# Optimization experiments

Hardware: AMD Instinct MI355X
Metric: run time of the kernel (lower is better)

Reference implementation:

```python
import jax, jax.numpy as jnp
import numpy as np

HIDDEN = 512

def setup_inputs() -> dict:
    key = jax.random.key(0)
    ks = jax.random.split(key, 6)
    B, T = 65536, 100
    scale = 0.1  # keep tanh MLP in a sane dynamic range
    return {
        "y0": jax.random.normal(ks[0], (B, 2), jnp.float32),
        "t_points": jnp.arange(T, dtype=jnp.float32) * 0.01,
        "W1": jax.random.normal(ks[1], (2, HIDDEN), jnp.float32) * scale,
        "b1": jnp.zeros((HIDDEN,), jnp.float32),
        "W2": jax.random.normal(ks[2], (HIDDEN, HIDDEN), jnp.float32) * scale,
        "b2": jnp.zeros((HIDDEN,), jnp.float32),
        "W3": jax.random.normal(ks[3], (HIDDEN, HIDDEN // 2), jnp.float32) * scale,
        "b3": jnp.zeros((HIDDEN // 2,), jnp.float32),
        "W4": jax.random.normal(ks[4], (HIDDEN // 2, 2), jnp.float32) * scale,
        "b4": jnp.zeros((2,), jnp.float32),
    }

def _mlp(y, W1, b1, W2, b2, W3, b3, W4, b4):
    # 4-layer tanh MLP: 2 -> H -> H -> H//2 -> 2 (t is unused in ODEFunc)
    h = jnp.tanh(y @ W1 + b1)
    h = jnp.tanh(h @ W2 + b2)
    h = jnp.tanh(h @ W3 + b3)
    return h @ W4 + b4

def reference(y0, t_points, W1, b1, W2, b2, W3, b3, W4, b4):
    f = lambda y: _mlp(y, W1, b1, W2, b2, W3, b3, W4, b4)
    dts = t_points[1:] - t_points[:-1]  # [T-1]

    def step(y, dt):
        k1 = f(y)
        k2 = f(y + k1 * (dt * 0.5))
        k3 = f(y + k2 * (dt * 0.5))
        k4 = f(y + k3 * dt)
        y_next = y + (dt / 6.0) * (k1 + 2.0 * k2 + 2.0 * k3 + k4)
        return y_next, y_next

    _, traj = jax.lax.scan(step, y0, dts)
    return jnp.concatenate([y0[None], traj], axis=0)  # [T, B, 2]
```

## Files before the change

### kernel.cpp

```cpp
#include <hip/hip_runtime.h>
#include <hip/hip_bf16.h>
#include <stdint.h>

using bfrag_t = __attribute__((ext_vector_type(8))) short;
using f32x16  = __attribute__((ext_vector_type(16))) float;

#define HID  512
#define H3   256
#define RB   64
#define NTH  512
#define KSC  2.885390081777927f

static __device__ __forceinline__ uint32_t bf16_rne(float f) {
    uint32_t u = __float_as_uint(f);
    return (u + 0x7fffu + ((u >> 16) & 1u)) >> 16;
}
static __device__ __forceinline__ uint32_t pk_bf16(float a, float b) {
    union { __hip_bfloat162 h; uint32_t u; } c;
    c.h = __float22bfloat162_rn(make_float2(a, b));
    return c.u;
}
static __device__ __forceinline__ float fast_exp2(float x) {
#if __has_builtin(__builtin_amdgcn_exp2f)
    return __builtin_amdgcn_exp2f(x);
#else
    return exp2f(x);
#endif
}
static __device__ __forceinline__ float fast_rcp(float x) {
#if __has_builtin(__builtin_amdgcn_rcpf)
    return __builtin_amdgcn_rcpf(x);
#else
    return 1.0f / x;
#endif
}
static __device__ __forceinline__ float ftanh_s(float xs) {
    float e = fast_exp2(xs);
    return 1.0f - 2.0f * fast_rcp(e + 1.0f);
}
static __device__ __forceinline__ bfrag_t frag_of(uint4 v) {
    union { uint4 u; bfrag_t f; } c; c.u = v; return c.f;
}

__global__ void prep_weights(const float* __restrict__ W1, const float* __restrict__ b1,
                             const float* __restrict__ W2, const float* __restrict__ b2,
                             const float* __restrict__ W3, const float* __restrict__ b3,
                             uint4* __restrict__ o2, uint4* __restrict__ o3,
                             float* __restrict__ w1p, float* __restrict__ b2s,
                             float* __restrict__ b3s)
{
    int id = blockIdx.x * 256 + threadIdx.x;
    if (id < 32768) {
        int l = id & 63, kt = (id >> 6) & 31, mt = id >> 11;
        int m = mt * 32 + (l & 31), k0 = kt * 16 + (l >> 5) * 8;
        uint32_t p[4];
        #pragma unroll
        for (int jj = 0; jj < 4; ++jj) {
            float v0 = KSC * W2[(k0 + jj * 2    ) * 512 + m];
            float v1 = KSC * W2[(k0 + jj * 2 + 1) * 512 + m];
            p[jj] = bf16_rne(v0) | (bf16_rne(v1) << 16);
        }
        o2[id] = make_uint4(p[0], p[1], p[2], p[3]);
    } else if (id < 49152) {
        int id2 = id - 32768;
        int l = id2 & 63, kt = (id2 >> 6) & 31, mt = id2 >> 11;
        int m = mt * 32 + (l & 31), k0 = kt * 16 + (l >> 5) * 8;
        uint32_t p[4];
        #pragma unroll
        for (int jj = 0; jj < 4; ++jj) {
            float v0 = KSC * W3[(k0 + jj * 2    ) * 256 + m];
            float v1 = KSC * W3[(k0 + jj * 2 + 1) * 256 + m];
            p[jj] = bf16_rne(v0) | (bf16_rne(v1) << 16);
        }
        o3[id2] = make_uint4(p[0], p[1], p[2], p[3]);
    } else if (id < 49152 + 1536) {
        int t = id - 49152;
        int ck = t / 24, j = t % 24;
        int f = ck * 8 + (j & 7);
        float v = (j < 8) ? W1[f] : (j < 16) ? W1[512 + f] : b1[f];
        w1p[t] = KSC * v;
    } else if (id < 49152 + 1536 + 512) {
        int i = id - 49152 - 1536; b2s[i] = KSC * b2[i];
    } else if (id < 49152 + 1536 + 512 + 256) {
        int i = id - 49152 - 1536 - 512; b3s[i] = KSC * b3[i];
    }
}

struct SmemT {
    uint4  hbuf[64 * RB];
    float  b2[HID];
    float  b3[H3];
    float  y [RB][2];
    float  z [RB][2];
    float  ya[RB][2];
    float  part[8][RB][2];
};

__global__ __launch_bounds__(NTH, 4) void node_kernel(
    const float* __restrict__ y0, const float* __restrict__ tp,
    const float* __restrict__ W4g, const float* __restrict__ b4g,
    const uint4* __restrict__ w2A, const uint4* __restrict__ w3A,
    const float* __restrict__ w1p, const float* __restrict__ b2s,
    const float* __restrict__ b3s,
    float* __restrict__ out, int Bn, int T)
{
    __shared__ SmemT s;
    const int tid = threadIdx.x;
    const int l   = tid & 63;
    const int w   = tid >> 6;
    const int wu  = __builtin_amdgcn_readfirstlane(w);
    const int b0  = blockIdx.x * RB;
    const int ln  = l & 31, lh = l >> 5;

    for (int i = tid; i < HID; i += NTH) s.b2[i] = b2s[i];
    for (int i = tid; i < H3;  i += NTH) s.b3[i] = b3s[i];
    if (tid < RB) {
        float2 v = ((const float2*)y0)[b0 + tid];
        s.y [tid][0] = v.x; s.y [tid][1] = v.y;
        s.z [tid][0] = v.x; s.z [tid][1] = v.y;
        s.ya[tid][0] = v.x; s.ya[tid][1] = v.y;
        ((float2*)out)[b0 + tid] = v;
    }
    __syncthreads();

    const float* w1w = w1p + wu * 8 * 24;
    const uint4* pW2 = w2A + (wu * 64) * 64 + l;
    const uint4* pW3 = w3A + (wu * 32) * 64 + l;

    for (int st = 0; st < T - 1; ++st) {
        float dt = tp[st + 1] - tp[st];

        for (int e = 0; e < 4; ++e) {
            uint4 aC[2], aN[2];
            aC[0] = pW2[0];           aC[1] = pW2[32 * 64];
            aN[0] = pW2[64];          aN[1] = pW2[32 * 64 + 64];

            {
                float zl0 = s.z[l][0], zl1 = s.z[l][1];
                #pragma unroll
                for (int i = 0; i < 8; ++i) {
                    const float* P = w1w + i * 24;
                    int ck = wu * 8 + i;
                    float xa[8];
                    #pragma unroll
                    for (int jj = 0; jj < 8; ++jj) {
                        float wa = P[jj], wb = P[8 + jj], bb = P[16 + jj];
                        xa[jj] = ftanh_s(fmaf(zl0, wa, fmaf(zl1, wb, bb)));
                    }
                    s.hbuf[ck * RB + l] = make_uint4(
                        pk_bf16(xa[0], xa[1]), pk_bf16(xa[2], xa[3]),
                        pk_bf16(xa[4], xa[5]), pk_bf16(xa[6], xa[7]));
                }
            }
            __syncthreads();

            uint4 a3C, a3N;
            {
                f32x16 acc[2][2];
                #pragma unroll
                for (int mt = 0; mt < 2; ++mt) {
                    int mb = (wu * 2 + mt) * 32 + 4 * lh;
                    float bv[16];
                    *(float4*)&bv[0]  = *(const float4*)&s.b2[mb];
                    *(float4*)&bv[4]  = *(const float4*)&s.b2[mb + 8];
                    *(float4*)&bv[8]  = *(const float4*)&s.b2[mb + 16];
                    *(float4*)&bv[12] = *(const float4*)&s.b2[mb + 24];
                    f32x16 a;
                    #pragma unroll
                    for (int r = 0; r < 16; ++r) a[r] = bv[r];
                    #pragma unroll
                    for (int nt = 0; nt < 2; ++nt) acc[mt][nt] = a;
                }
                #pragma unroll 2
                for (int kt = 0; kt < 32; ++kt) {
                    uint4 bF[2];
                    #pragma unroll
                    for (int nt = 0; nt < 2; ++nt)
                        bF[nt] = s.hbuf[(kt * 2 + lh) * RB + nt * 32 + ln];
                    int kq = (kt < 30) ? (kt + 2) : 29;
                    uint4 aM0 = pW2[kq * 64];
                    uint4 aM1 = pW2[32 * 64 + kq * 64];
                    #pragma unroll
                    for (int mt = 0; mt < 2; ++mt)
                        #pragma unroll
                        for (int nt = 0; nt < 2; ++nt)
                            acc[mt][nt] = __builtin_amdgcn_mfma_f32_32x32x16_bf16(
                                frag_of(aC[mt]), frag_of(bF[nt]), acc[mt][nt], 0, 0, 0);
                    aC[0] = aN[0]; aC[1] = aN[1];
                    aN[0] = aM0;   aN[1] = aM1;
                }
                a3C = pW3[0];      a3N = pW3[64];
                __syncthreads();
                #pragma unroll
                for (int mt = 0; mt < 2; ++mt) {
                    int m0 = (wu * 2 + mt) * 32 + 4 * lh;
                    int hi = lh;
                    #pragma unroll
                    for (int nt = 0; nt < 2; ++nt) {
                        int n = nt * 32 + ln;
                        f32x16 c = acc[mt][nt];
                        #pragma unroll
                        for (int g = 0; g < 4; ++g) {
                            int ck = (m0 + 8 * g) >> 3;
                            uint32_t u0 = pk_bf16(ftanh_s(c[4 * g    ]), ftanh_s(c[4 * g + 1]));
                            uint32_t u1 = pk_bf16(ftanh_s(c[4 * g + 2]), ftanh_s(c[4 * g + 3]));
                            ((uint2*)s.hbuf)[((ck * RB + n) << 1) | hi] = make_uint2(u0, u1);
                        }
                    }
                }
                __syncthreads();
            }

            {
                f32x16 acc3[2];
                {
                    int mb = wu * 32 + 4 * lh;
                    float bv[16];
                    *(float4*)&bv[0]  = *(const float4*)&s.b3[mb];
                    *(float4*)&bv[4]  = *(const float4*)&s.b3[mb + 8];
                    *(float4*)&bv[8]  = *(const float4*)&s.b3[mb + 16];
                    *(float4*)&bv[12] = *(const float4*)&s.b3[mb + 24];
                    f32x16 a;
                    #pragma unroll
                    for (int r = 0; r < 16; ++r) a[r] = bv[r];
                    acc3[0] = a; acc3[1] = a;
                }
                #pragma unroll 2
                for (int kt = 0; kt < 32; ++kt) {
                    uint4 bF[2];
                    #pragma unroll
                    for (int nt = 0; nt < 2; ++nt)
                        bF[nt] = s.hbuf[(kt * 2 + lh) * RB + nt * 32 + ln];
                    int kq = (kt < 30) ? (kt + 2) : 29;
                    uint4 aM = pW3[kq * 64];
                    #pragma unroll
                    for (int nt = 0; nt < 2; ++nt)
                        acc3[nt] = __builtin_amdgcn_mfma_f32_32x32x16_bf16(
                            frag_of(a3C), frag_of(bF[nt]), acc3[nt], 0, 0, 0);
                    a3C = a3N; a3N = aM;
                }
                __syncthreads();
                {
                    int m0 = wu * 32 + 4 * lh;
                    int hi = lh;
                    #pragma unroll
                    for (int nt = 0; nt < 2; ++nt) {
                        int n = nt * 32 + ln;
                        f32x16 c = acc3[nt];
                        #pragma unroll
                        for (int g = 0; g < 4; ++g) {
                            int ck = (m0 + 8 * g) >> 3;
                            uint32_t u0 = pk_bf16(ftanh_s(c[4 * g    ]), ftanh_s(c[4 * g + 1]));
                            uint32_t u1 = pk_bf16(ftanh_s(c[4 * g + 2]), ftanh_s(c[4 * g + 3]));
                            ((uint2*)s.hbuf)[((ck * RB + n) << 1) | hi] = make_uint2(u0, u1);
                        }
                    }
                }
                __syncthreads();
            }

            {
                int r  = l;
                int qq = wu;
                float a0 = 0.f, a1 = 0.f;
                #pragma unroll
                for (int j = 0; j < 4; ++j) {
                    int ck = qq * 4 + j;
                    uint4 hv = s.hbuf[ck * RB + r];
                    const uint32_t* pu = (const uint32_t*)&hv;
                    #pragma unroll
                    for (int jj = 0; jj < 4; ++jj) {
                        uint32_t uu = pu[jj];
                        float h0 = __uint_as_float(uu << 16);
                        float h1 = __uint_as_float(uu & 0xffff0000u);
                        int f = ck * 8 + jj * 2;
                        a0 = fmaf(h0, W4g[f * 2],     fmaf(h1, W4g[f * 2 + 2], a0));
                        a1 = fmaf(h0, W4g[f * 2 + 1], fmaf(h1, W4g[f * 2 + 3], a1));
                    }
                }
                s.part[qq][r][0] = a0; s.part[qq][r][1] = a1;
            }
            __syncthreads();

            if (tid < RB) {
                float k0 = b4g[0], k1 = b4g[1];
                #pragma unroll
                for (int p = 0; p < 8; ++p) {
                    k0 += s.part[p][tid][0];
                    k1 += s.part[p][tid][1];
                }
                float wg = (e == 0 || e == 3) ? dt * (1.f / 6.f) : dt * (1.f / 3.f);
                float ya0 = s.ya[tid][0] + wg * k0;
                float ya1 = s.ya[tid][1] + wg * k1;
                s.ya[tid][0] = ya0; s.ya[tid][1] = ya1;
                if (e < 3) {
                    float aa = (e == 2) ? dt : dt * 0.5f;
                    s.z[tid][0] = s.y[tid][0] + aa * k0;
                    s.z[tid][1] = s.y[tid][1] + aa * k1;
                } else {
                    s.y[tid][0] = ya0; s.y[tid][1] = ya1;
                    s.z[tid][0] = ya0; s.z[tid][1] = ya1;
                    ((float2*)out)[(size_t)(st + 1) * Bn + b0 + tid] =
                        make_float2(ya0, ya1);
                }
            }
            __syncthreads();
        }
    }
}

extern "C" void kernel_launch(void* const* d_in, const int* in_sizes, int n_in,
                              void* d_out, int out_size, void* d_ws, size_t ws_size,
                              hipStream_t stream)
{
    const float* y0 = (const float*)d_in[0];
    const float* tp = (const float*)d_in[1];
    const float* W1 = (const float*)d_in[2];
    const float* b1 = (const float*)d_in[3];
    const float* W2 = (const float*)d_in[4];
    const float* b2 = (const float*)d_in[5];
    const float* W3 = (const float*)d_in[6];
    const float* b3 = (const float*)d_in[7];
    const float* W4 = (const float*)d_in[8];
    const float* b4 = (const float*)d_in[9];
    float* out = (float*)d_out;

    const int Bn = in_sizes[0] / 2;
    const int T  = in_sizes[1];

    uint4* w2A = (uint4*)d_ws;
    uint4* w3A = w2A + 32768;
    float* w1p = (float*)(w3A + 16384);
    float* b2s = w1p + 1536;
    float* b3s = b2s + 512;

    prep_weights<<<201, 256, 0, stream>>>(W1, b1, W2, b2, W3, b3,
                                          w2A, w3A, w1p, b2s, b3s);
    node_kernel<<<Bn / RB, NTH, 0, stream>>>(y0, tp, W4, b4,
                                             w2A, w3A, w1p, b2s, b3s, out, Bn, T);
}
```

Baseline: 26.77 ms.

## Double rows per block with 16 waves split into M and N groups

Raises the per-block batch tile from 64 to 128 rows and threads from 512 to 1024. Waves are split into an M group (weight rows) and an N group (two 64-row halves of the batch), so each streamed W2/W3 fragment from global/L2 is reused across twice as many rows. This costs a larger shared-memory footprint and fewer resident blocks, and the launch bounds of 4 blocks at 1024 threads may force register spilling. The SmemT sizes and the unseen tail code must also match the new RB.

```diff
diff --git a/kernel.cpp b/kernel.cpp
--- a/kernel.cpp
+++ b/kernel.cpp
@@ -7,8 +7,8 @@
 
 #define HID  512
 #define H3   256
-#define RB   64
-#define NTH  512
+#define RB   128
+#define NTH  1024
 #define KSC  2.885390081777927f
 
 static __device__ __forceinline__ uint32_t bf16_rne(float f) {
@@ -111,6 +111,7 @@
     const int wu  = __builtin_amdgcn_readfirstlane(w);
     const int b0  = blockIdx.x * RB;
     const int ln  = l & 31, lh = l >> 5;
+    const int mg  = wu >> 1, ng = wu & 1;
 
     for (int i = tid; i < HID; i += NTH) s.b2[i] = b2s[i];
     for (int i = tid; i < H3;  i += NTH) s.b3[i] = b3s[i];
@@ -123,33 +124,38 @@
     }
     __syncthreads();
 
-    const float* w1w = w1p + wu * 8 * 24;
-    const uint4* pW2 = w2A + (wu * 64) * 64 + l;
-    const uint4* pW3 = w3A + (wu * 32) * 64 + l;
+    const float* w1w = w1p + wu * 4 * 24;
+    const uint4* pW2 = w2A + (mg * 2) * 2048 + l;
+    const uint4* pW3 = w3A + mg * 2048 + l;
 
     for (int st = 0; st < T - 1; ++st) {
         float dt = tp[st + 1] - tp[st];
 
         for (int e = 0; e < 4; ++e) {
             uint4 aC[2], aN[2];
-            aC[0] = pW2[0];           aC[1] = pW2[32 * 64];
-            aN[0] = pW2[64];          aN[1] = pW2[32 * 64 + 64];
+            aC[0] = pW2[0];           aC[1] = pW2[2048];
+            aN[0] = pW2[64];          aN[1] = pW2[2048 + 64];
 
             {
-                float zl0 = s.z[l][0], zl1 = s.z[l][1];
-                #pragma unroll
-                for (int i = 0; i < 8; ++i) {
+                float zl0 = s.z[l][0],      zl1 = s.z[l][1];
+                float zh0 = s.z[64 + l][0], zh1 = s.z[64 + l][1];
+                #pragma unroll
+                for (int i = 0; i < 4; ++i) {
                     const float* P = w1w + i * 24;
-                    int ck = wu * 8 + i;
-                    float xa[8];
+                    int ck = wu * 4 + i;
+                    float xa[8], xb[8];
                     #pragma unroll
                     for (int jj = 0; jj < 8; ++jj) {
                         float wa = P[jj], wb = P[8 + jj], bb = P[16 + jj];
                         xa[jj] = ftanh_s(fmaf(zl0, wa, fmaf(zl1, wb, bb)));
+                        xb[jj] = ftanh_s(fmaf(zh0, wa, fmaf(zh1, wb, bb)));
                     }
                     s.hbuf[ck * RB + l] = make_uint4(
                         pk_bf16(xa[0], xa[1]), pk_bf16(xa[2], xa[3]),
                         pk_bf16(xa[4], xa[5]), pk_bf16(xa[6], xa[7]));
+                    s.hbuf[ck * RB + 64 + l] = make_uint4(
+                        pk_bf16(xb[0], xb[1]), pk_bf16(xb[2], xb[3]),
+                        pk_bf16(xb[4], xb[5]), pk_bf16(xb[6], xb[7]));
                 }
             }
             __syncthreads();
@@ -159,7 +165,7 @@
                 f32x16 acc[2][2];
                 #pragma unroll
                 for (int mt = 0; mt < 2; ++mt) {
-                    int mb = (wu * 2 + mt) * 32 + 4 * lh;
+                    int mb = (mg * 2 + mt) * 32 + 4 * lh;
                     float bv[16];
                     *(float4*)&bv[0]  = *(const float4*)&s.b2[mb];
                     *(float4*)&bv[4]  = *(const float4*)&s.b2[mb + 8];
@@ -176,10 +182,10 @@
                     uint4 bF[2];
                     #pragma unroll
                     for (int nt = 0; nt < 2; ++nt)
-                        bF[nt] = s.hbuf[(kt * 2 + lh) * RB + nt * 32 + ln];
+                        bF[nt] = s.hbuf[(kt * 2 + lh) * RB + ng * 64 + nt * 32 + ln];
                     int kq = (kt < 30) ? (kt + 2) : 29;
                     uint4 aM0 = pW2[kq * 64];
-                    uint4 aM1 = pW2[32 * 64 + kq * 64];
+                    uint4 aM1 = pW2[2048 + kq * 64];
                     #pragma unroll
                     for (int mt = 0; mt < 2; ++mt)
                         #pragma unroll
@@ -193,11 +199,11 @@
                 __syncthreads();
                 #pragma unroll
                 for (int mt = 0; mt < 2; ++mt) {
-                    int m0 = (wu * 2 + mt) * 32 + 4 * lh;
+                    int m0 = (mg * 2 + mt) * 32 + 4 * lh;
                     int hi = lh;
                     #pragma unroll
                     for (int nt = 0; nt < 2; ++nt) {
-                        int n = nt * 32 + ln;
+                        int n = ng * 64 + nt * 32 + ln;
                         f32x16 c = acc[mt][nt];
                         #pragma unroll
                         for (int g = 0; g < 4; ++g) {
@@ -214,7 +220,7 @@
             {
                 f32x16 acc3[2];
                 {
-                    int mb = wu * 32 + 4 * lh;
+                    int mb = mg * 32 + 4 * lh;
                     float bv[16];
                     *(float4*)&bv[0]  = *(const float4*)&s.b3[mb];
                     *(float4*)&bv[4]  = *(const float4*)&s.b3[mb + 8];
@@ -230,7 +236,7 @@
                     uint4 bF[2];
                     #pragma unroll
                     for (int nt = 0; nt < 2; ++nt)
-                        bF[nt] = s.hbuf[(kt * 2 + lh) * RB + nt * 32 + ln];
+                        bF[nt] = s.hbuf[(kt * 2 + lh) * RB + ng * 64 + nt * 32 + ln];
                     int kq = (kt < 30) ? (kt + 2) : 29;
                     uint4 aM = pW3[kq * 64];
                     #pragma unroll
@@ -241,11 +247,11 @@
                 }
                 __syncthreads();
                 {
-                    int m0 = wu * 32 + 4 * lh;
+                    int m0 = mg * 32 + 4 * lh;
                     int hi = lh;
                     #pragma unroll
                     for (int nt = 0; nt < 2; ++nt) {
-                        int n = nt * 32 + ln;
+                        int n = ng * 64 + nt * 32 + ln;
                         f32x16 c = acc3[nt];
                         #pragma unroll
                         for (int g = 0; g < 4; ++g) {
@@ -260,8 +266,8 @@
             }
 
             {
-                int r  = l;
-                int qq = wu;
+                int r  = tid & 127;
+                int qq = __builtin_amdgcn_readfirstlane(tid >> 7);
                 float a0 = 0.f, a1 = 0.f;
                 #pragma unroll
                 for (int j = 0; j < 4; ++j) {
```

Result: no change. 26.57 ms (-0.8%).

## Process two 64-row halves per block, overlapping tanh epilogues with MFMA loops

Applied to the files above, without the earlier changes.

Each block now handles 128 batch rows split into two 64-row halves with separate hbuf regions. The layer-1 tanh, layer-2 epilogue and layer-3 epilogue of one half are interleaved with the MFMA k-loop of the other half, so transcendental work overlaps matrix work and fewer barriers are needed per row. Layer 4 is fused directly into the layer-3 accumulator epilogue using a permuted W4 held in shared memory, which removes an hbuf round trip. Register pressure doubles, so launch bounds drop to 2 blocks per CU, and occupancy may fall.

```diff
diff --git a/kernel.cpp b/kernel.cpp
--- a/kernel.cpp
+++ b/kernel.cpp
@@ -7,7 +7,7 @@
 
 #define HID  512
 #define H3   256
-#define RB   64
+#define RB   128
 #define NTH  512
 #define KSC  2.885390081777927f
 
@@ -45,9 +45,10 @@
 __global__ void prep_weights(const float* __restrict__ W1, const float* __restrict__ b1,
                              const float* __restrict__ W2, const float* __restrict__ b2,
                              const float* __restrict__ W3, const float* __restrict__ b3,
+                             const float* __restrict__ W4,
                              uint4* __restrict__ o2, uint4* __restrict__ o3,
                              float* __restrict__ w1p, float* __restrict__ b2s,
-                             float* __restrict__ b3s)
+                             float* __restrict__ b3s, float* __restrict__ w4f)
 {
     int id = blockIdx.x * 256 + threadIdx.x;
     if (id < 32768) {
@@ -83,25 +84,34 @@
         int i = id - 49152 - 1536; b2s[i] = KSC * b2[i];
     } else if (id < 49152 + 1536 + 512 + 256) {
         int i = id - 49152 - 1536 - 512; b3s[i] = KSC * b3[i];
+    } else if (id < 49152 + 1536 + 512 + 256 + 512) {
+        int t = id - (49152 + 1536 + 512 + 256);
+        int c  = t & 1;
+        int r  = (t >> 1) & 15;
+        int lh = (t >> 5) & 1;
+        int wv = t >> 6;
+        int m = wv * 32 + (r & 3) + 8 * (r >> 2) + 4 * lh;
+        w4f[t] = W4[m * 2 + c];
     }
 }
 
 struct SmemT {
-    uint4  hbuf[64 * RB];
+    uint4  hbuf[8192];
     float  b2[HID];
     float  b3[H3];
+    float  w4[512];
     float  y [RB][2];
     float  z [RB][2];
     float  ya[RB][2];
-    float  part[8][RB][2];
+    float  part[16][RB][2];
 };
 
-__global__ __launch_bounds__(NTH, 4) void node_kernel(
+__global__ __launch_bounds__(NTH, 2) void node_kernel(
     const float* __restrict__ y0, const float* __restrict__ tp,
-    const float* __restrict__ W4g, const float* __restrict__ b4g,
+    const float* __restrict__ b4g,
     const uint4* __restrict__ w2A, const uint4* __restrict__ w3A,
     const float* __restrict__ w1p, const float* __restrict__ b2s,
-    const float* __restrict__ b3s,
+    const float* __restrict__ b3s, const float* __restrict__ w4f,
     float* __restrict__ out, int Bn, int T)
 {
     __shared__ SmemT s;
@@ -114,6 +124,7 @@
 
     for (int i = tid; i < HID; i += NTH) s.b2[i] = b2s[i];
     for (int i = tid; i < H3;  i += NTH) s.b3[i] = b3s[i];
+    if (tid < 512) s.w4[tid] = w4f[tid];
     if (tid < RB) {
         float2 v = ((const float2*)y0)[b0 + tid];
         s.y [tid][0] = v.x; s.y [tid][1] = v.y;
@@ -126,166 +137,239 @@
     const float* w1w = w1p + wu * 8 * 24;
     const uint4* pW2 = w2A + (wu * 64) * 64 + l;
     const uint4* pW3 = w3A + (wu * 32) * 64 + l;
+    const float* w4l = &s.w4[(wu * 2 + lh) * 32];
 
     for (int st = 0; st < T - 1; ++st) {
         float dt = tp[st + 1] - tp[st];
 
         for (int e = 0; e < 4; ++e) {
-            uint4 aC[2], aN[2];
-            aC[0] = pW2[0];           aC[1] = pW2[32 * 64];
-            aN[0] = pW2[64];          aN[1] = pW2[32 * 64 + 64];
+            uint4 aC0 = pW2[0], aC1 = pW2[2048];
+            uint4 aN0 = pW2[64], aN1 = pW2[2048 + 64];
 
             {
-                float zl0 = s.z[l][0], zl1 = s.z[l][1];
+                float za0 = s.z[l][0], za1 = s.z[l][1];
                 #pragma unroll
                 for (int i = 0; i < 8; ++i) {
                     const float* P = w1w + i * 24;
                     int ck = wu * 8 + i;
                     float xa[8];
                     #pragma unroll
-                    for (int jj = 0; jj < 8; ++jj) {
-                        float wa = P[jj], wb = P[8 + jj], bb = P[16 + jj];
-                        xa[jj] = ftanh_s(fmaf(zl0, wa, fmaf(zl1, wb, bb)));
-                    }
-                    s.hbuf[ck * RB + l] = make_uint4(
+                    for (int jj = 0; jj < 8; ++jj)
+                        xa[jj] = ftanh_s(fmaf(za0, P[jj], fmaf(za1, P[8 + jj], P[16 + jj])));
+                    s.hbuf[ck * 64 + l] = make_uint4(
                         pk_bf16(xa[0], xa[1]), pk_bf16(xa[2], xa[3]),
                         pk_bf16(xa[4], xa[5]), pk_bf16(xa[6], xa[7]));
                 }
             }
             __syncthreads();
 
-            uint4 a3C, a3N;
+            f32x16 accA[2][2];
+            #pragma unroll
+            for (int mt = 0; mt < 2; ++mt) {
+                int mb = (wu * 2 + mt) * 32 + 4 * lh;
+                float bv[16];
+                *(float4*)&bv[0]  = *(const float4*)&s.b2[mb];
+                *(float4*)&bv[4]  = *(const float4*)&s.b2[mb + 8];
+                *(float4*)&bv[8]  = *(const float4*)&s.b2[mb + 16];
+                *(float4*)&bv[12] = *(const float4*)&s.b2[mb + 24];
+                f32x16 a;
+                #pragma unroll
+                for (int r = 0; r < 16; ++r) a[r] = bv[r];
+                accA[mt][0] = a; accA[mt][1] = a;
+            }
             {
-                f32x16 acc[2][2];
-                #pragma unroll
-                for (int mt = 0; mt < 2; ++mt) {
-                    int mb = (wu * 2 + mt) * 32 + 4 * lh;
-                    float bv[16];
-                    *(float4*)&bv[0]  = *(const float4*)&s.b2[mb];
-                    *(float4*)&bv[4]  = *(const float4*)&s.b2[mb + 8];
-                    *(float4*)&bv[8]  = *(const float4*)&s.b2[mb + 16];
-                    *(float4*)&bv[12] = *(const float4*)&s.b2[mb + 24];
-                    f32x16 a;
+                float zb0 = s.z[64 + l][0], zb1 = s.z[64 + l][1];
+                #pragma unroll
+                for (int q = 0; q < 8; ++q) {
+                    {
+                        const float* P = w1w + q * 24;
+                        int ck = wu * 8 + q;
+                        float xb[8];
+                        #pragma unroll
+                        for (int jj = 0; jj < 8; ++jj)
+                            xb[jj] = ftanh_s(fmaf(zb0, P[jj], fmaf(zb1, P[8 + jj], P[16 + jj])));
+                        s.hbuf[4096 + ck * 64 + l] = make_uint4(
+                            pk_bf16(xb[0], xb[1]), pk_bf16(xb[2], xb[3]),
+                            pk_bf16(xb[4], xb[5]), pk_bf16(xb[6], xb[7]));
+                    }
                     #pragma unroll
-                    for (int r = 0; r < 16; ++r) a[r] = bv[r];
+                    for (int k4 = 0; k4 < 4; ++k4) {
+                        int kt = q * 4 + k4;
+                        uint4 bF0 = s.hbuf[(kt * 2 + lh) * 64 + ln];
+                        uint4 bF1 = s.hbuf[(kt * 2 + lh) * 64 + 32 + ln];
+                        int kq = (kt < 30) ? (kt + 2) : 29;
+                        uint4 aM0 = pW2[kq * 64];
+                        uint4 aM1 = pW2[2048 + kq * 64];
+                        accA[0][0] = __builtin_amdgcn_mfma_f32_32x32x16_bf16(
+                            frag_of(aC0), frag_of(bF0), accA[0][0], 0, 0, 0);
+                        accA[0][1] = __builtin_amdgcn_mfma_f32_32x32x16_bf16(
+                            frag_of(aC0), frag_of(bF1), accA[0][1], 0, 0, 0);
+                        accA[1][0] = __builtin_amdgcn_mfma_f32_32x32x16_bf16(
+                            frag_of(aC1), frag_of(bF0), accA[1][0], 0, 0, 0);
+                        accA[1][1] = __builtin_amdgcn_mfma_f32_32x32x16_bf16(
+                            frag_of(aC1), frag_of(bF1), accA[1][1], 0, 0, 0);
+                        aC0 = aN0; aC1 = aN1; aN0 = aM0; aN1 = aM1;
+                    }
+                }
+            }
+            aC0 = pW2[0]; aC1 = pW2[2048];
+            aN0 = pW2[64]; aN1 = pW2[2048 + 64];
+            __syncthreads();
+
+            f32x16 accB[2][2];
+            #pragma unroll
+            for (int mt = 0; mt < 2; ++mt) {
+                int mb = (wu * 2 + mt) * 32 + 4 * lh;
+                float bv[16];
+                *(float4*)&bv[0]  = *(const float4*)&s.b2[mb];
+                *(float4*)&bv[4]  = *(const float4*)&s.b2[mb + 8];
+                *(float4*)&bv[8]  = *(const float4*)&s.b2[mb + 16];
+                *(float4*)&bv[12] = *(const float4*)&s.b2[mb + 24];
+                f32x16 a;
+                #pragma unroll
+                for (int r = 0; r < 16; ++r) a[r] = bv[r];
+                accB[mt][0] = a; accB[mt][1] = a;
+            }
+            #pragma unroll
+            for (int q4 = 0; q4 < 4; ++q4) {
+                int emt = q4 >> 1, ent = q4 & 1;
+                {
+                    int m0 = (wu * 2 + emt) * 32 + 4 * lh;
+                    int n  = ent * 32 + ln;
+                    f32x16 c = accA[emt][ent];
                     #pragma unroll
-                    for (int nt = 0; nt < 2; ++nt) acc[mt][nt] = a;
-                }
-                #pragma unroll 2
-                for (int kt = 0; kt < 32; ++kt) {
-                    uint4 bF[2];
-                    #pragma unroll
-                    for (int nt = 0; nt < 2; ++nt)
-                        bF[nt] = s.hbuf[(kt * 2 + lh) * RB + nt * 32 + ln];
+                    for (int g = 0; g < 4; ++g) {
+                        int ck = (m0 + 8 * g) >> 3;
+                        uint32_t u0 = pk_bf16(ftanh_s(c[4 * g    ]), ftanh_s(c[4 * g + 1]));
+                        uint32_t u1 = pk_bf16(ftanh_s(c[4 * g + 2]), ftanh_s(c[4 * g + 3]));
+                        ((uint2*)s.hbuf)[((ck * 64 + n) << 1) | lh] = make_uint2(u0, u1);
+                    }
+                }
+                #pragma unroll
+                for (int k8 = 0; k8 < 8; ++k8) {
+                    int kt = q4 * 8 + k8;
+                    uint4 bF0 = s.hbuf[4096 + (kt * 2 + lh) * 64 + ln];
+                    uint4 bF1 = s.hbuf[4096 + (kt * 2 + lh) * 64 + 32 + ln];
                     int kq = (kt < 30) ? (kt + 2) : 29;
                     uint4 aM0 = pW2[kq * 64];
-                    uint4 aM1 = pW2[32 * 64 + kq * 64];
+                    uint4 aM1 = pW2[2048 + kq * 64];
+                    accB[0][0] = __builtin_amdgcn_mfma_f32_32x32x16_bf16(
+                        frag_of(aC0), frag_of(bF0), accB[0][0], 0, 0, 0);
+                    accB[0][1] = __builtin_amdgcn_mfma_f32_32x32x16_bf16(
+                        frag_of(aC0), frag_of(bF1), accB[0][1], 0, 0, 0);
+                    accB[1][0] = __builtin_amdgcn_mfma_f32_32x32x16_bf16(
+                        frag_of(aC1), frag_of(bF0), accB[1][0], 0, 0, 0);
+                    accB[1][1] = __builtin_amdgcn_mfma_f32_32x32x16_bf16(
+                        frag_of(aC1), frag_of(bF1), accB[1][1], 0, 0, 0);
+                    aC0 = aN0; aC1 = aN1; aN0 = aM0; aN1 = aM1;
+                }
+            }
+            uint4 c3C = pW3[0], c3N = pW3[64];
+            __syncthreads();
+
+            f32x16 acc3A[2];
+            {
+                int mb = wu * 32 + 4 * lh;
+                float bv[16];
+                *(float4*)&bv[0]  = *(const float4*)&s.b3[mb];
+                *(float4*)&bv[4]  = *(const float4*)&s.b3[mb + 8];
+                *(float4*)&bv[8]  = *(const float4*)&s.b3[mb + 16];
+                *(float4*)&bv[12] = *(const float4*)&s.b3[mb + 24];
+                f32x16 a;
+                #pragma unroll
+                for (int r = 0; r < 16; ++r) a[r] = bv[r];
+                acc3A[0] = a; acc3A[1] = a;
+            }
+            #pragma unroll
+            for (int q4 = 0; q4 < 4; ++q4) {
+                int emt = q4 >> 1, ent = q4 & 1;
+                {
+                    int m0 = (wu * 2 + emt) * 32 + 4 * lh;
+                    int n  = ent * 32 + ln;
+                    f32x16 c = accB[emt][ent];
                     #pragma unroll
-                    for (int mt = 0; mt < 2; ++mt)
-                        #pragma unroll
-                        for (int nt = 0; nt < 2; ++nt)
-                            acc[mt][nt] = __builtin_amdgcn_mfma_f32_32x32x16_bf16(
-                                frag_of(aC[mt]), frag_of(bF[nt]), acc[mt][nt], 0, 0, 0);
-                    aC[0] = aN[0]; aC[1] = aN[1];
-                    aN[0] = aM0;   aN[1] = aM1;
-                }
-                a3C = pW3[0];      a3N = pW3[64];
-                __syncthreads();
-                #pragma unroll
-                for (int mt = 0; mt < 2; ++mt) {
-                    int m0 = (wu * 2 + mt) * 32 + 4 * lh;
-                    int hi = lh;
-                    #pragma unroll
-                    for (int nt = 0; nt < 2; ++nt) {
-                        int n = nt * 32 + ln;
-                        f32x16 c = acc[mt][nt];
-                        #pragma unroll
-                        for (int g = 0; g < 4; ++g) {
-                            int ck = (m0 + 8 * g) >> 3;
-                            uint32_t u0 = pk_bf16(ftanh_s(c[4 * g    ]), ftanh_s(c[4 * g + 1]));
-                            uint32_t u1 = pk_bf16(ftanh_s(c[4 * g + 2]), ftanh_s(c[4 * g + 3]));
-                            ((uint2*)s.hbuf)[((ck * RB + n) << 1) | hi] = make_uint2(u0, u1);
-                        }
+                    for (int g = 0; g < 4; ++g) {
+                        int ck = (m0 + 8 * g) >> 3;
+                        uint32_t u0 = pk_bf16(ftanh_s(c[4 * g    ]), ftanh_s(c[4 * g + 1]));
+                        uint32_t u1 = pk_bf16(ftanh_s(c[4 * g + 2]), ftanh_s(c[4 * g + 3]));
+                        ((uint2*)s.hbuf)[((4096 + ck * 64 + n) << 1) | lh] = make_uint2(u0, u1);
                     }
                 }
-                __syncthreads();
-            }
-
-            {
-                f32x16 acc3[2];
-                {
-                    int mb = wu * 32 + 4 * lh;
-                    float bv[16];
-                    *(float4*)&bv[0]  = *(const float4*)&s.b3[mb];
-                    *(float4*)&bv[4]  = *(const float4*)&s.b3[mb + 8];
-                    *(float4*)&bv[8]  = *(const float4*)&s.b3[mb + 16];
-                    *(float4*)&bv[12] = *(const float4*)&s.b3[mb + 24];
-                    f32x16 a;
-                    #pragma unroll
-                    for (int r = 0; r < 16; ++r) a[r] = bv[r];
-                    acc3[0] = a; acc3[1] = a;
-                }
-                #pragma unroll 2
-                for (int kt = 0; kt < 32; ++kt) {
-                    uint4 bF[2];
-                    #pragma unroll
-                    for (int nt = 0; nt < 2; ++nt)
-                        bF[nt] = s.hbuf[(kt * 2 + lh) * RB + nt * 32 + ln];
+                #pragma unroll
+                for (int k8 = 0; k8 < 8; ++k8) {
+                    int kt = q4 * 8 + k8;
+                    uint4 bF0 = s.hbuf[(kt * 2 + lh) * 64 + ln];
+                    uint4 bF1 = s.hbuf[(kt * 2 + lh) * 64 + 32 + ln];
                     int kq = (kt < 30) ? (kt + 2) : 29;
                     uint4 aM = pW3[kq * 64];
+                    acc3A[0] = __builtin_amdgcn_mfma_f32_32x32x16_bf16(
+                        frag_of(c3C), frag_of(bF0), acc3A[0], 0, 0, 0);
+                    acc3A[1] = __builtin_amdgcn_mfma_f32_32x32x16_bf16(
+                        frag_of(c3C), frag_of(bF1), acc3A[1], 0, 0, 0);
+                    c3C = c3N; c3N = aM;
+                }
+            }
+            c3C = pW3[0]; c3N = pW3[64];
+            __syncthreads();
+
+            f32x16 acc3B[2];
+            {
+                int mb = wu * 32 + 4 * lh;
+                float bv[16];
+                *(float4*)&bv[0]  = *(const float4*)&s.b3[mb];
+                *(float4*)&bv[4]  = *(const float4*)&s.b3[mb + 8];
+                *(float4*)&bv[8]  = *(const float4*)&s.b3[mb + 16];
+                *(float4*)&bv[12] = *(const float4*)&s.b3[mb + 24];
+                f32x16 a;
+                #pragma unroll
+                for (int r = 0; r < 16; ++r) a[r] = bv[r];
+                acc3B[0] = a; acc3B[1] = a;
+            }
+            #pragma unroll
+            for (int h2 = 0; h2 < 2; ++h2) {
+                {
+                    float p0 = 0.f, p1 = 0.f;
                     #pragma unroll
-                    for (int nt = 0; nt < 2; ++nt)
-                        acc3[nt] = __builtin_amdgcn_mfma_f32_32x32x16_bf16(
-                            frag_of(a3C), frag_of(bF[nt]), acc3[nt], 0, 0, 0);
-                    a3C = a3N; a3N = aM;
-                }
-                __syncthreads();
-                {
-                    int m0 = wu * 32 + 4 * lh;
-                    int hi = lh;
-                    #pragma unroll
-                    for (int nt = 0; nt < 2; ++nt) {
-                        int n = nt * 32 + ln;
-                        f32x16 c = acc3[nt];
-                        #pragma unroll
-                        for (int g = 0; g < 4; ++g) {
-                            int ck = (m0 + 8 * g) >> 3;
-                            uint32_t u0 = pk_bf16(ftanh_s(c[4 * g    ]), ftanh_s(c[4 * g + 1]));
-                            uint32_t u1 = pk_bf16(ftanh_s(c[4 * g + 2]), ftanh_s(c[4 * g + 3]));
-                            ((uint2*)s.hbuf)[((ck * RB + n) << 1) | hi] = make_uint2(u0, u1);
-                        }
+                    for (int r = 0; r < 16; ++r) {
+                        float hh = ftanh_s(acc3A[h2][r]);
+                        p0 = fmaf(hh, w4l[r * 2],     p0);
+                        p1 = fmaf(hh, w4l[r * 2 + 1], p1);
                     }
-                }
-                __syncthreads();
-            }
-
-            {
-                int r  = l;
-                int qq = wu;
-                float a0 = 0.f, a1 = 0.f;
-                #pragma unroll
-                for (int j = 0; j < 4; ++j) {
-                    int ck = qq * 4 + j;
-                    uint4 hv = s.hbuf[ck * RB + r];
-                    const uint32_t* pu = (const uint32_t*)&hv;
-                    #pragma unroll
-                    for (int jj = 0; jj < 4; ++jj) {
-                        uint32_t uu = pu[jj];
-                        float h0 = __uint_as_float(uu << 16);
-                        float h1 = __uint_as_float(uu & 0xffff0000u);
-                        int f = ck * 8 + jj * 2;
-                        a0 = fmaf(h0, W4g[f * 2],     fmaf(h1, W4g[f * 2 + 2], a0));
-                        a1 = fmaf(h0, W4g[f * 2 + 1], fmaf(h1, W4g[f * 2 + 3], a1));
-                    }
-                }
-                s.part[qq][r][0] = a0; s.part[qq][r][1] = a1;
+                    s.part[wu * 2 + lh][h2 * 32 + ln][0] = p0;
+                    s.part[wu * 2 + lh][h2 * 32 + ln][1] = p1;
+                }
+                #pragma unroll
+                for (int k16 = 0; k16 < 16; ++k16) {
+                    int kt = h2 * 16 + k16;
+                    uint4 bF0 = s.hbuf[4096 + (kt * 2 + lh) * 64 + ln];
+                    uint4 bF1 = s.hbuf[4096 + (kt * 2 + lh) * 64 + 32 + ln];
+                    int kq = (kt < 30) ? (kt + 2) : 29;
+                    uint4 aM = pW3[kq * 64];
+                    acc3B[0] = __builtin_amdgcn_mfma_f32_32x32x16_bf16(
+                        frag_of(c3C), frag_of(bF0), acc3B[0], 0, 0, 0);
+                    acc3B[1] = __builtin_amdgcn_mfma_f32_32x32x16_bf16(
+                        frag_of(c3C), frag_of(bF1), acc3B[1], 0, 0, 0);
+                    c3C = c3N; c3N = aM;
+                }
+            }
+            #pragma unroll
+            for (int nt = 0; nt < 2; ++nt) {
+                float p0 = 0.f, p1 = 0.f;
+                #pragma unroll
+                for (int r = 0; r < 16; ++r) {
+                    float hh = ftanh_s(acc3B[nt][r]);
+                    p0 = fmaf(hh, w4l[r * 2],     p0);
+                    p1 = fmaf(hh, w4l[r * 2 + 1], p1);
+                }
+                s.part[wu * 2 + lh][64 + nt * 32 + ln][0] = p0;
+                s.part[wu * 2 + lh][64 + nt * 32 + ln][1] = p1;
             }
             __syncthreads();
 
             if (tid < RB) {
                 float k0 = b4g[0], k1 = b4g[1];
                 #pragma unroll
-                for (int p = 0; p < 8; ++p) {
+                for (int p = 0; p < 16; ++p) {
                     k0 += s.part[p][tid][0];
                     k1 += s.part[p][tid][1];
                 }
@@ -333,9 +417,11 @@
     float* w1p = (float*)(w3A + 16384);
     float* b2s = w1p + 1536;
     float* b3s = b2s + 512;
-
-    prep_weights<<<201, 256, 0, stream>>>(W1, b1, W2, b2, W3, b3,
-                                          w2A, w3A, w1p, b2s, b3s);
-    node_kernel<<<Bn / RB, NTH, 0, stream>>>(y0, tp, W4, b4,
-                                             w2A, w3A, w1p, b2s, b3s, out, Bn, T);
-}
+    float* w4f = b3s + 256;
+
+    prep_weights<<<204, 256, 0, stream>>>(W1, b1, W2, b2, W3, b3, W4,
+                                          w2A, w3A, w1p, b2s, b3s, w4f);
+    node_kernel<<<Bn / RB, NTH, 0, stream>>>(y0, tp, b4,
+                                             w2A, w3A, w1p, b2s, b3s, w4f,
+                                             out, Bn, T);
+}
```

Result: slower. 52.60 ms (+96.5%).
